# Optimization experiments

Hardware: AMD Instinct MI355X
Metric: run time of the kernel (lower is better)

Reference implementation:

```python
import jax, jax.numpy as jnp
import numpy as np

B, L, D = 2, 2048, 1024
H = 16          # num_heads == num_key_value_heads
FD = 16         # feature_dim (q/k head dim)
HD = D // H     # head_dim = 64 (v head dim)
EPS = 1e-5


def setup_inputs() -> dict:
    key = jax.random.key(0)
    k0, k1, k2, k3, k4 = jax.random.split(key, 5)
    scale = 0.02
    return {
        "hidden_states": jax.random.normal(k0, (B, L, D), jnp.float32),
        "Wq": jax.random.normal(k1, (D, H * FD), jnp.float32) * scale,
        "Wk": jax.random.normal(k2, (D, H * FD), jnp.float32) * scale,
        "Wv": jax.random.normal(k3, (D, H * HD), jnp.float32) * scale,
        "Wo": jax.random.normal(k4, (H * HD, D), jnp.float32) * scale,
    }


def reference(hidden_states, Wq, Wk, Wv, Wo):
    # projections (bias-free), split heads: b l (h d) -> b h l d
    q = (hidden_states @ Wq).reshape(B, L, H, FD).transpose(0, 2, 1, 3)
    k = (hidden_states @ Wk).reshape(B, L, H, FD).transpose(0, 2, 1, 3)
    v = (hidden_states @ Wv).reshape(B, L, H, HD).transpose(0, 2, 1, 3)

    # parallel_rebased: squared-dot-product kernel attention, causal,
    # row-normalized by the kernel sum (use_scale=True, use_normalize=True)
    qk_scale = FD ** -0.5
    s = jnp.einsum('bhqd,bhkd->bhqk', q * qk_scale, k)
    s = s * s  # quadratic feature map: (q.k)^2
    causal = jnp.tril(jnp.ones((L, L), dtype=bool))
    s = jnp.where(causal, s, 0.0)
    z = jnp.sum(s, axis=-1)  # [B,H,L]
    o = jnp.einsum('bhqk,bhkd->bhqd', s, v) / (z[..., None] + EPS)

    # merge heads: b h l d -> b l (h d), output projection
    o = o.transpose(0, 2, 1, 3).reshape(B, L, H * HD)
    return o @ Wo
```

## Files before the change

### kernel.cpp

```cpp
#include <hip/hip_runtime.h>
#include <hip/hip_bf16.h>

#define BB 2
#define LL 2048
#define DD 1024
#define HH 16
#define FD 16
#define HD 64
#define EPS 1e-5f
#define RQKV 1536
#define NFIX 4

typedef __attribute__((ext_vector_type(4))) float f32x4;
typedef __attribute__((ext_vector_type(8))) _Float16 f16x8;
typedef __attribute__((ext_vector_type(4))) _Float16 f16x4;
typedef __attribute__((ext_vector_type(4))) unsigned int u32x4;

__global__ __launch_bounds__(256) void prep(
    const float* __restrict__ Wq, const float* __restrict__ Wk,
    const float* __restrict__ Wv, const float* __restrict__ Wo,
    const float* __restrict__ hs, _Float16* __restrict__ WqkvT,
    _Float16* __restrict__ WoT, float* __restrict__ QKVe,
    _Float16* __restrict__ HS16) {
  __shared__ __attribute__((aligned(16))) char smem[40960];
  const int bx = blockIdx.x;
  const int tid = threadIdx.x;

  if (bx >= 2608) {
    int idx = ((bx - 2608) * 256 + tid) * 16;
#pragma unroll
    for (int half = 0; half < 2; half++) {
      float4 a = *(const float4*)(hs + idx + half * 8);
      float4 b = *(const float4*)(hs + idx + half * 8 + 4);
      f16x8 p = {(_Float16)a.x, (_Float16)a.y, (_Float16)a.z, (_Float16)a.w,
                 (_Float16)b.x, (_Float16)b.y, (_Float16)b.z, (_Float16)b.w};
      *(f16x8*)(HS16 + idx + half * 8) = p;
    }
    return;
  }

  if (bx < 2560) {
    _Float16(*s)[40] = (_Float16(*)[40])smem;
    const float* src;
    _Float16* dst;
    int n0, ncol, drow, k0;
    if (bx < 1536) {
      int ct = bx % 48, kt = bx / 48;
      if (ct < 8) { src = Wq; n0 = ct * 32; ncol = 256; drow = n0; }
      else if (ct < 16) { src = Wk; n0 = (ct - 8) * 32; ncol = 256; drow = 256 + n0; }
      else { src = Wv; n0 = (ct - 16) * 32; ncol = 1024; drow = 512 + n0; }
      k0 = kt * 32;
      dst = WqkvT;
    } else {
      int i2 = bx - 1536;
      n0 = (i2 & 31) * 32; k0 = (i2 >> 5) * 32;
      src = Wo; ncol = DD; drow = n0; dst = WoT;
    }
    {
      int r = tid >> 3, c = (tid & 7) * 4;
      float4 v = *(const float4*)(src + (size_t)(k0 + r) * ncol + n0 + c);
      f16x4 p = {(_Float16)v.x, (_Float16)v.y, (_Float16)v.z, (_Float16)v.w};
      *(f16x4*)&s[r][c] = p;
    }
    __syncthreads();
    {
      int n = tid >> 3, kk = (tid & 7) * 4;
      f16x4 o = {s[kk + 0][n], s[kk + 1][n], s[kk + 2][n], s[kk + 3][n]};
      *(f16x4*)(dst + (size_t)(drow + n) * DD + k0 + kk) = o;
    }
    return;
  }

  float(*sHS)[DD] = (float(*)[DD])smem;
  float(*part)[8][32] = (float(*)[8][32])(smem + 32768);
  const int kg = tid >> 5, c = tid & 31;
  const int c0 = (bx - 2560) * 32;

  for (int i = tid; i < 8 * (DD / 4); i += 256) {
    int e = i / (DD / 4), col4 = (i % (DD / 4)) * 4;
    int b = e >> 2, r = e & 3;
    *(float4*)&sHS[e][col4] =
        *(const float4*)(hs + (size_t)(b * LL + r) * DD + col4);
  }
  __syncthreads();

  const float* W;
  int col, ncol;
  if (c0 < 256) { W = Wq; col = c0 + c; ncol = 256; }
  else if (c0 < 512) { W = Wk; col = (c0 - 256) + c; ncol = 256; }
  else { W = Wv; col = (c0 - 512) + c; ncol = 1024; }

  float acc[8] = {};
  const int d0 = kg * 128;
#pragma unroll 4
  for (int d = d0; d < d0 + 128; d++) {
    float wv = W[(size_t)d * ncol + col];
#pragma unroll
    for (int e = 0; e < 8; e++) acc[e] += sHS[e][d] * wv;
  }
#pragma unroll
  for (int e = 0; e < 8; e++) part[kg][e][c] = acc[e];
  __syncthreads();

  {
    int e = tid >> 5;
    float t = 0.f;
#pragma unroll
    for (int g = 0; g < 8; g++) t += part[g][e][c];
    QKVe[(size_t)e * RQKV + c0 + c] = t;
  }
}

template <typename OutT>
__global__ __launch_bounds__(256) void gemm_f16(
    const _Float16* __restrict__ A, const _Float16* __restrict__ Bt,
    OutT* __restrict__ C, int M, int N, int K) {
  __shared__ __attribute__((aligned(16))) _Float16 sA[128 * 64];
  __shared__ __attribute__((aligned(16))) _Float16 sB[64 * 64];
  const int tid = threadIdx.x;
  const int m0 = blockIdx.y * 128, n0 = blockIdx.x * 64;
  const int w = tid >> 6, lane = tid & 63, quad = lane >> 4, l16 = lane & 15;
  const int wm = (w >> 1) * 64, wn = (w & 1) * 32;

  const int sr = tid >> 1, p = tid & 1;
  const int brow = (tid & 127) >> 1;
  const _Float16* Ag = A + (size_t)(m0 + sr) * K + p * 32;
  const _Float16* Bg = Bt + (size_t)(n0 + brow) * K + p * 32;
  _Float16* sAw = &sA[sr * 64];
  _Float16* sBw = &sB[brow * 64];
  const int aswz = sr & 7, bswz = brow & 7;

  f32x4 acc[4][2];
#pragma unroll
  for (int i = 0; i < 4; i++)
#pragma unroll
    for (int j = 0; j < 2; j++) acc[i][j] = (f32x4){0.f, 0.f, 0.f, 0.f};

  f16x8 ar[4], br[4];
  auto LOAD = [&](int k0) {
#pragma unroll
    for (int i = 0; i < 4; i++) ar[i] = *(const f16x8*)(Ag + k0 + i * 8);
    if (tid < 128) {
#pragma unroll
      for (int i = 0; i < 4; i++) br[i] = *(const f16x8*)(Bg + k0 + i * 8);
    }
  };
  LOAD(0);

  for (int k0 = 0; k0 < K; k0 += 64) {
    __syncthreads();
#pragma unroll
    for (int i = 0; i < 4; i++)
      *(f16x8*)(sAw + (((4 * p + i) ^ aswz) * 8)) = ar[i];
    if (tid < 128) {
#pragma unroll
      for (int i = 0; i < 4; i++)
        *(f16x8*)(sBw + (((4 * p + i) ^ bswz) * 8)) = br[i];
    }
    __syncthreads();
    if (k0 + 64 < K) LOAD(k0 + 64);

#pragma unroll
    for (int s = 0; s < 2; s++) {
      f16x8 af[4], bf[2];
#pragma unroll
      for (int i = 0; i < 4; i++) {
        int row = wm + i * 16 + l16;
        int col = ((s * 4 + quad) ^ (row & 7)) * 8;
        af[i] = *(const f16x8*)&sA[row * 64 + col];
      }
#pragma unroll
      for (int j = 0; j < 2; j++) {
        int row = wn + j * 16 + l16;
        int col = ((s * 4 + quad) ^ (row & 7)) * 8;
        bf[j] = *(const f16x8*)&sB[row * 64 + col];
      }
#pragma unroll
      for (int i = 0; i < 4; i++)
#pragma unroll
        for (int j = 0; j < 2; j++)
          acc[i][j] = __builtin_amdgcn_mfma_f32_16x16x32_f16(af[i], bf[j], acc[i][j], 0, 0, 0);
    }
  }

#pragma unroll
  for (int i = 0; i < 4; i++)
#pragma unroll
    for (int j = 0; j < 2; j++)
#pragma unroll
      for (int r = 0; r < 4; r++) {
        const int row = m0 + wm + i * 16 + quad * 4 + r;
        const int col = n0 + wn + j * 16 + l16;
        C[(size_t)row * N + col] = (OutT)acc[i][j][r];
      }
}

__device__ __forceinline__ unsigned pack_f16x2(float a, float b) {
  unsigned short ua = __builtin_bit_cast(unsigned short, (_Float16)a);
  unsigned short ub = __builtin_bit_cast(unsigned short, (_Float16)b);
  return (unsigned)ua | ((unsigned)ub << 16);
}

#define SK5 24
#define SV5 136

__global__ __launch_bounds__(256, 5) void attn_mfma7(
    const _Float16* __restrict__ QKV, _Float16* __restrict__ O) {
  __shared__ __attribute__((aligned(16))) _Float16 sK[128 * SK5];
  __shared__ __attribute__((aligned(16))) _Float16 sVt[80 * SV5];

  const int bh = blockIdx.x;
  const int b = bh >> 4, h = bh & 15;
  const int qt = 31 - blockIdx.y;
  const int tid = threadIdx.x;
  const int w = tid >> 6;
  const int lane = tid & 63;
  const int quad = lane >> 4;
  const int l16 = lane & 15;
  const int gq = qt * 64 + w * 16;

  const int pc = (lane & 32) | ((lane & 12) << 1) | ((lane & 16) >> 2) | (lane & 3);

  f16x8 qfrag = {};
  if (quad < 2) {
    qfrag = *(const f16x8*)(QKV +
        (size_t)(b * LL + gq + l16) * RQKV + h * FD + quad * 8);
    const _Float16 RT2 = (_Float16)1.41421356f;
#pragma unroll
    for (int i = 0; i < 8; i++) qfrag[i] = qfrag[i] * RT2;
  }

  for (int t = tid; t < 16 * SV5; t += 256) {
    int r = t / SV5, c = t % SV5;
    sVt[64 * SV5 + t] = (_Float16)((r == 0 && c < 128) ? 1.0f : 0.0f);
  }
  __syncthreads();
  const f16x8 zf0 = *(const f16x8*)&sVt[(64 + l16) * SV5 + quad * 8];
  const f16x8 zf1 = *(const f16x8*)&sVt[(64 + l16) * SV5 + 32 + quad * 8];

  f32x4 oacc[4];
  f32x4 zacc = (f32x4){0.f, 0.f, 0.f, 0.f};
#pragma unroll
  for (int nt = 0; nt < 4; nt++) oacc[nt] = (f32x4){0.f, 0.f, 0.f, 0.f};

  const int nst = qt + 1;
  const int nkt = (nst + 1) >> 1;

  const int krow = tid >> 1, kcol = (tid & 1) * 8;
  f16x8 kreg;
  f16x8 vreg0, vreg1, vreg2, vreg3;
  auto LOAD = [&](int kt) {
    kreg = *(const f16x8*)(QKV +
        (size_t)(b * LL + kt * 128 + krow) * RQKV + 256 + h * FD + kcol);
    const _Float16* vp = QKV +
        (size_t)(b * LL + kt * 128 + lane) * RQKV + 512 + h * HD + w * 16;
    vreg0 = *(const f16x8*)vp;
    vreg1 = *(const f16x8*)(vp + 8);
    vp += (size_t)64 * RQKV;
    vreg2 = *(const f16x8*)vp;
    vreg3 = *(const f16x8*)(vp + 8);
  };
  LOAD(0);

  for (int kt = 0; kt < nkt; kt++) {
    __syncthreads();
    *(f16x8*)&sK[krow * SK5 + kcol] = kreg;
#pragma unroll
    for (int t = 0; t < 8; t++) sVt[(w * 16 + t) * SV5 + pc] = vreg0[t];
#pragma unroll
    for (int t = 0; t < 8; t++) sVt[(w * 16 + 8 + t) * SV5 + pc] = vreg1[t];
#pragma unroll
    for (int t = 0; t < 8; t++) sVt[(w * 16 + t) * SV5 + 64 + pc] = vreg2[t];
#pragma unroll
    for (int t = 0; t < 8; t++) sVt[(w * 16 + 8 + t) * SV5 + 64 + pc] = vreg3[t];
    __syncthreads();
    if (kt + 1 < nkt) LOAD(kt + 1);

#pragma unroll
    for (int hf = 0; hf < 2; hf++) {
      const int st = 2 * kt + hf;
      if (st >= nst) break;
      const int k0 = st * 64;
      const bool mask = (st == qt);

      f16x8 kf[4];
#pragma unroll
      for (int nt = 0; nt < 4; nt++) {
        f16x8 f = {};
        if (quad < 2)
          f = *(const f16x8*)&sK[(hf * 64 + nt * 16 + l16) * SK5 + quad * 8];
        kf[nt] = f;
      }

      unsigned wp[4][2];
#pragma unroll
      for (int nt = 0; nt < 4; nt++) {
        f32x4 s = __builtin_amdgcn_mfma_f32_16x16x32_f16(
            kf[nt], qfrag, (f32x4){0.f, 0.f, 0.f, 0.f}, 0, 0, 0);
        float s0 = s[0] * s[0], s1 = s[1] * s[1];
        float s2 = s[2] * s[2], s3 = s[3] * s[3];
        if (mask) {
          const int gkb = k0 + nt * 16 + quad * 4;
          const int qg = gq + l16;
          if (gkb + 0 > qg) s0 = 0.f;
          if (gkb + 1 > qg) s1 = 0.f;
          if (gkb + 2 > qg) s2 = 0.f;
          if (gkb + 3 > qg) s3 = 0.f;
        }
        wp[nt][0] = pack_f16x2(s0, s1);
        wp[nt][1] = pack_f16x2(s2, s3);
      }

      u32x4 u0 = {wp[0][0], wp[0][1], wp[1][0], wp[1][1]};
      u32x4 u1 = {wp[2][0], wp[2][1], wp[3][0], wp[3][1]};
      f16x8 af0 = __builtin_bit_cast(f16x8, u0);
      f16x8 af1 = __builtin_bit_cast(f16x8, u1);

#pragma unroll
      for (int nt = 0; nt < 4; nt++) {
        f16x8 vf0 = *(const f16x8*)&sVt[(nt * 16 + l16) * SV5 + hf * 64 + quad * 8];
        f16x8 vf1 = *(const f16x8*)&sVt[(nt * 16 + l16) * SV5 + hf * 64 + 32 + quad * 8];
        oacc[nt] = __builtin_amdgcn_mfma_f32_16x16x32_f16(af0, vf0, oacc[nt], 0, 0, 0);
        oacc[nt] = __builtin_amdgcn_mfma_f32_16x16x32_f16(af1, vf1, oacc[nt], 0, 0, 0);
      }
      zacc = __builtin_amdgcn_mfma_f32_16x16x32_f16(af0, zf0, zacc, 0, 0, 0);
      zacc = __builtin_amdgcn_mfma_f32_16x16x32_f16(af1, zf1, zacc, 0, 0, 0);
    }
  }

  {
    float rz[4];
#pragma unroll
    for (int r = 0; r < 4; r++) {
      float zz = __shfl(zacc[r], lane & 48);
      rz[r] = 1.0f / (zz + 32.0f * EPS);
    }
#pragma unroll
    for (int nt = 0; nt < 4; nt++)
#pragma unroll
      for (int r = 0; r < 4; r++) {
        const int gqr = gq + quad * 4 + r;
        O[(size_t)(b * LL + gqr) * (HH * HD) + h * HD + nt * 16 + l16] =
            (_Float16)(oacc[nt][r] * rz[r]);
      }
  }
}

__global__ __launch_bounds__(256) void fix_final(
    const float* __restrict__ QKVe, _Float16* __restrict__ Oatt) {
  const int b = blockIdx.x >> 4, h = blockIdx.x & 15;
  const int tid = threadIdx.x;
  const int p = tid >> 6, d = tid & 63;

  float num = 0.f, z = 0.f;
  const float* qrow = QKVe + (size_t)(b * 4 + p) * RQKV + h * FD;
  for (int j = 0; j <= p; j++) {
    const float* krow = QKVe + (size_t)(b * 4 + j) * RQKV + 256 + h * FD;
    float s = 0.f;
#pragma unroll
    for (int f = 0; f < FD; f++) s += qrow[f] * krow[f];
    s *= 0.25f;
    s = s * s;
    z += s;
    num += s * QKVe[(size_t)(b * 4 + j) * RQKV + 512 + h * HD + d];
  }
  Oatt[(size_t)(b * LL + p) * (HH * HD) + h * HD + d] =
      (_Float16)(num / (z + EPS));
}

extern "C" void kernel_launch(void* const* d_in, const int* in_sizes, int n_in,
                              void* d_out, int out_size, void* d_ws, size_t ws_size,
                              hipStream_t stream) {
  const float* hs = (const float*)d_in[0];
  const float* Wq = (const float*)d_in[1];
  const float* Wk = (const float*)d_in[2];
  const float* Wv = (const float*)d_in[3];
  const float* Wo = (const float*)d_in[4];
  float* out = (float*)d_out;

  char* ws = (char*)d_ws;
  _Float16* WqkvT = (_Float16*)ws;
  _Float16* WoT   = (_Float16*)(ws + (3ull << 20));
  _Float16* HS16  = (_Float16*)(ws + (5ull << 20));
  _Float16* QKV   = (_Float16*)(ws + (13ull << 20));
  _Float16* Oatt  = (_Float16*)(ws + (25ull << 20));
  float*    QKVe  = (float*)(ws + (33ull << 20));

  const int M = BB * LL;

  prep<<<dim3(3632), 256, 0, stream>>>(Wq, Wk, Wv, Wo, hs, WqkvT, WoT, QKVe, HS16);

  gemm_f16<_Float16><<<dim3(RQKV / 64, M / 128), 256, 0, stream>>>(
      HS16, WqkvT, QKV, M, RQKV, DD);

  attn_mfma7<<<dim3(BB * HH, LL / 64), 256, 0, stream>>>(QKV, Oatt);

  fix_final<<<dim3(BB * HH), 256, 0, stream>>>(QKVe, Oatt);

  gemm_f16<float><<<dim3(DD / 64, M / 128), 256, 0, stream>>>(
      Oatt, WoT, out, M, DD, DD);
}
```

Baseline: 165.7 us.

## Pre-transpose V into a separate buffer so attention stores it to LDS with vector writes

Adds a `vtrans` kernel that transposes the V slice of the fused QKV buffer into a feature-major VT layout in workspace. The attention kernel then reads V rows that are already transposed and writes them to LDS with 8-byte stores through a permutation table. Previously each thread did 32 scalar 2-byte scattered LDS stores per tile. The aim is to cut LDS store instruction count and bank pressure in the attention main loop, at the cost of an extra kernel launch and an extra global read and write pass over V.

```diff
diff --git a/kernel.cpp b/kernel.cpp
--- a/kernel.cpp
+++ b/kernel.cpp
@@ -195,6 +195,34 @@
       }
 }
 
+__global__ __launch_bounds__(256) void vtrans(
+    const _Float16* __restrict__ QKV, _Float16* __restrict__ VT) {
+  __shared__ __attribute__((aligned(16))) _Float16 s[64][136];
+  const int h = blockIdx.x >> 5, tt = blockIdx.x & 31;
+  const int tid = threadIdx.x;
+
+  {
+    const int tok = tid >> 1, dh = (tid & 1) * 32;
+    const _Float16* src =
+        QKV + (size_t)(tt * 128 + tok) * RQKV + 512 + h * HD + dh;
+    f16x8 r[4];
+#pragma unroll
+    for (int i = 0; i < 4; i++) r[i] = *(const f16x8*)(src + i * 8);
+#pragma unroll
+    for (int i = 0; i < 4; i++)
+#pragma unroll
+      for (int e = 0; e < 8; e++) s[dh + i * 8 + e][tok] = r[i][e];
+  }
+  __syncthreads();
+  {
+    const int d = tid >> 2, ck = (tid & 3) * 32;
+    _Float16* dst = VT + (size_t)(h * HD + d) * (BB * LL) + tt * 128 + ck;
+#pragma unroll
+    for (int i = 0; i < 4; i++)
+      *(f16x8*)(dst + i * 8) = *(const f16x8*)&s[d][ck + i * 8];
+  }
+}
+
 __device__ __forceinline__ unsigned pack_f16x2(float a, float b) {
   unsigned short ua = __builtin_bit_cast(unsigned short, (_Float16)a);
   unsigned short ub = __builtin_bit_cast(unsigned short, (_Float16)b);
@@ -204,8 +232,9 @@
 #define SK5 24
 #define SV5 136
 
-__global__ __launch_bounds__(256, 5) void attn_mfma7(
-    const _Float16* __restrict__ QKV, _Float16* __restrict__ O) {
+__global__ __launch_bounds__(256, 5) void attn_mfma8(
+    const _Float16* __restrict__ QKV, const _Float16* __restrict__ VT,
+    _Float16* __restrict__ O) {
   __shared__ __attribute__((aligned(16))) _Float16 sK[128 * SK5];
   __shared__ __attribute__((aligned(16))) _Float16 sVt[80 * SV5];
 
@@ -219,8 +248,6 @@
   const int l16 = lane & 15;
   const int gq = qt * 64 + w * 16;
 
-  const int pc = (lane & 32) | ((lane & 12) << 1) | ((lane & 16) >> 2) | (lane & 3);
-
   f16x8 qfrag = {};
   if (quad < 2) {
     qfrag = *(const f16x8*)(QKV +
@@ -247,32 +274,36 @@
   const int nkt = (nst + 1) >> 1;
 
   const int krow = tid >> 1, kcol = (tid & 1) * 8;
+  const int vdrow = w * 16 + (lane >> 2);
+  const int vc0 = (lane & 3) * 32;
+  const _Float16* VTb =
+      VT + (size_t)(h * HD + vdrow) * (BB * LL) + b * LL + vc0;
   f16x8 kreg;
-  f16x8 vreg0, vreg1, vreg2, vreg3;
+  f16x8 vreg[4];
   auto LOAD = [&](int kt) {
     kreg = *(const f16x8*)(QKV +
         (size_t)(b * LL + kt * 128 + krow) * RQKV + 256 + h * FD + kcol);
-    const _Float16* vp = QKV +
-        (size_t)(b * LL + kt * 128 + lane) * RQKV + 512 + h * HD + w * 16;
-    vreg0 = *(const f16x8*)vp;
-    vreg1 = *(const f16x8*)(vp + 8);
-    vp += (size_t)64 * RQKV;
-    vreg2 = *(const f16x8*)vp;
-    vreg3 = *(const f16x8*)(vp + 8);
+    const _Float16* vp = VTb + kt * 128;
+#pragma unroll
+    for (int i = 0; i < 4; i++) vreg[i] = *(const f16x8*)(vp + i * 8);
   };
   LOAD(0);
 
   for (int kt = 0; kt < nkt; kt++) {
     __syncthreads();
     *(f16x8*)&sK[krow * SK5 + kcol] = kreg;
-#pragma unroll
-    for (int t = 0; t < 8; t++) sVt[(w * 16 + t) * SV5 + pc] = vreg0[t];
-#pragma unroll
-    for (int t = 0; t < 8; t++) sVt[(w * 16 + 8 + t) * SV5 + pc] = vreg1[t];
-#pragma unroll
-    for (int t = 0; t < 8; t++) sVt[(w * 16 + t) * SV5 + 64 + pc] = vreg2[t];
-#pragma unroll
-    for (int t = 0; t < 8; t++) sVt[(w * 16 + 8 + t) * SV5 + 64 + pc] = vreg3[t];
+    {
+      _Float16* sv = &sVt[vdrow * SV5 + vc0];
+#pragma unroll
+      for (int a = 0; a < 8; a++) {
+        constexpr int tab[8] = {0, 8, 16, 24, 4, 12, 20, 28};
+        u32x4 u = __builtin_bit_cast(u32x4, vreg[a >> 1]);
+        uint2 val;
+        val.x = u[2 * (a & 1)];
+        val.y = u[2 * (a & 1) + 1];
+        *(uint2*)(sv + tab[a]) = val;
+      }
+    }
     __syncthreads();
     if (kt + 1 < nkt) LOAD(kt + 1);
 
@@ -385,6 +416,7 @@
   _Float16* QKV   = (_Float16*)(ws + (13ull << 20));
   _Float16* Oatt  = (_Float16*)(ws + (25ull << 20));
   float*    QKVe  = (float*)(ws + (33ull << 20));
+  _Float16* VT    = (_Float16*)(ws + (34ull << 20));
 
   const int M = BB * LL;
 
@@ -393,7 +425,9 @@
   gemm_f16<_Float16><<<dim3(RQKV / 64, M / 128), 256, 0, stream>>>(
       HS16, WqkvT, QKV, M, RQKV, DD);
 
-  attn_mfma7<<<dim3(BB * HH, LL / 64), 256, 0, stream>>>(QKV, Oatt);
+  vtrans<<<dim3(512), 256, 0, stream>>>(QKV, VT);
+
+  attn_mfma8<<<dim3(BB * HH, LL / 64), 256, 0, stream>>>(QKV, VT, Oatt);
 
   fix_final<<<dim3(BB * HH), 256, 0, stream>>>(QKVe, Oatt);
 
```

Measured after the change: 167.2 us. No clear change (+0.9%).

## Fuse first-rows attention fixup into output GEMM and reorder attention tiles

Applied to the files above, without the earlier changes.

Removes the separate fix_final launch. The first four rows of each batch are now computed inside the output projection GEMM, which writes them directly into the shared-memory A tile per k-chunk, so the fixup no longer needs an extra kernel and a global round trip. It also changes the query-tile ordering in the attention kernel to interleave heavy and light causal tiles, aiming for better load balance. The cost is extra work and an extra sync in the two GEMM row-blocks that hold batch starts.

```diff
diff --git a/kernel.cpp b/kernel.cpp
--- a/kernel.cpp
+++ b/kernel.cpp
@@ -111,16 +111,48 @@
   }
 }
 
-template <typename OutT>
+template <typename OutT, bool FIXA>
 __global__ __launch_bounds__(256) void gemm_f16(
     const _Float16* __restrict__ A, const _Float16* __restrict__ Bt,
-    OutT* __restrict__ C, int M, int N, int K) {
+    OutT* __restrict__ C, int M, int N, int K,
+    const float* __restrict__ QKVe) {
   __shared__ __attribute__((aligned(16))) _Float16 sA[128 * 64];
   __shared__ __attribute__((aligned(16))) _Float16 sB[64 * 64];
+  __shared__ float sfx2[FIXA ? 16 * 4 * 4 : 1];
+  __shared__ float sfxz[FIXA ? 16 * 4 : 1];
   const int tid = threadIdx.x;
   const int m0 = blockIdx.y * 128, n0 = blockIdx.x * 64;
   const int w = tid >> 6, lane = tid & 63, quad = lane >> 4, l16 = lane & 15;
   const int wm = (w >> 1) * 64, wn = (w & 1) * 32;
+
+  int fixb = -1;
+  if constexpr (FIXA) {
+    if (m0 == 0) fixb = 0;
+    else if (m0 == LL) fixb = 1;
+    if (fixb >= 0) {
+      const int hh = tid >> 4, u = tid & 15;
+      if (u < 10) {
+        const int p = (u < 1) ? 0 : (u < 3) ? 1 : (u < 6) ? 2 : 3;
+        const int j = u - p * (p + 1) / 2;
+        const float* qrow = QKVe + (size_t)(fixb * 4 + p) * RQKV + hh * FD;
+        const float* krow = QKVe + (size_t)(fixb * 4 + j) * RQKV + 256 + hh * FD;
+        float s = 0.f;
+#pragma unroll
+        for (int f = 0; f < FD; f++) s += qrow[f] * krow[f];
+        s *= 0.25f;
+        sfx2[(hh * 4 + p) * 4 + j] = s * s;
+      }
+      __syncthreads();
+      if (tid < 64) {
+        const int hh2 = tid >> 2, p = tid & 3;
+        float z = 0.f;
+#pragma unroll
+        for (int j = 0; j < 4; j++)
+          if (j <= p) z += sfx2[(hh2 * 4 + p) * 4 + j];
+        sfxz[hh2 * 4 + p] = z;
+      }
+    }
+  }
 
   const int sr = tid >> 1, p = tid & 1;
   const int brow = (tid & 127) >> 1;
@@ -129,6 +161,7 @@
   _Float16* sAw = &sA[sr * 64];
   _Float16* sBw = &sB[brow * 64];
   const int aswz = sr & 7, bswz = brow & 7;
+  const bool skipA = FIXA && fixb >= 0 && sr < 4;
 
   f32x4 acc[4][2];
 #pragma unroll
@@ -149,13 +182,31 @@
 
   for (int k0 = 0; k0 < K; k0 += 64) {
     __syncthreads();
-#pragma unroll
-    for (int i = 0; i < 4; i++)
-      *(f16x8*)(sAw + (((4 * p + i) ^ aswz) * 8)) = ar[i];
+    if (!skipA) {
+#pragma unroll
+      for (int i = 0; i < 4; i++)
+        *(f16x8*)(sAw + (((4 * p + i) ^ aswz) * 8)) = ar[i];
+    }
     if (tid < 128) {
 #pragma unroll
       for (int i = 0; i < 4; i++)
         *(f16x8*)(sBw + (((4 * p + i) ^ bswz) * 8)) = br[i];
+    }
+    if constexpr (FIXA) {
+      if (fixb >= 0) {
+        const int pp = tid >> 6, cc = tid & 63;
+        const int hh = k0 >> 6;
+        float num = 0.f;
+#pragma unroll
+        for (int j = 0; j < 4; j++)
+          if (j <= pp)
+            num = fmaf(sfx2[(hh * 4 + pp) * 4 + j],
+                       QKVe[(size_t)(fixb * 4 + j) * RQKV + 512 + k0 + cc],
+                       num);
+        const float zz = sfxz[hh * 4 + pp];
+        sA[pp * 64 + (((cc >> 3) ^ pp) * 8) + (cc & 7)] =
+            (_Float16)(num / (zz + EPS));
+      }
     }
     __syncthreads();
     if (k0 + 64 < K) LOAD(k0 + 64);
@@ -204,14 +255,16 @@
 #define SK5 24
 #define SV5 136
 
-__global__ __launch_bounds__(256, 5) void attn_mfma7(
+__global__ __launch_bounds__(256, 5) void attn_mfma9(
     const _Float16* __restrict__ QKV, _Float16* __restrict__ O) {
   __shared__ __attribute__((aligned(16))) _Float16 sK[128 * SK5];
   __shared__ __attribute__((aligned(16))) _Float16 sVt[80 * SV5];
 
   const int bh = blockIdx.x;
   const int b = bh >> 4, h = bh & 15;
-  const int qt = 31 - blockIdx.y;
+  const int y = blockIdx.y;
+  const int qt = (y < 8) ? (31 - y) : (y < 16) ? (y + 8)
+               : (y < 24) ? (31 - y) : (y - 24);
   const int tid = threadIdx.x;
   const int w = tid >> 6;
   const int lane = tid & 63;
@@ -346,28 +399,6 @@
   }
 }
 
-__global__ __launch_bounds__(256) void fix_final(
-    const float* __restrict__ QKVe, _Float16* __restrict__ Oatt) {
-  const int b = blockIdx.x >> 4, h = blockIdx.x & 15;
-  const int tid = threadIdx.x;
-  const int p = tid >> 6, d = tid & 63;
-
-  float num = 0.f, z = 0.f;
-  const float* qrow = QKVe + (size_t)(b * 4 + p) * RQKV + h * FD;
-  for (int j = 0; j <= p; j++) {
-    const float* krow = QKVe + (size_t)(b * 4 + j) * RQKV + 256 + h * FD;
-    float s = 0.f;
-#pragma unroll
-    for (int f = 0; f < FD; f++) s += qrow[f] * krow[f];
-    s *= 0.25f;
-    s = s * s;
-    z += s;
-    num += s * QKVe[(size_t)(b * 4 + j) * RQKV + 512 + h * HD + d];
-  }
-  Oatt[(size_t)(b * LL + p) * (HH * HD) + h * HD + d] =
-      (_Float16)(num / (z + EPS));
-}
-
 extern "C" void kernel_launch(void* const* d_in, const int* in_sizes, int n_in,
                               void* d_out, int out_size, void* d_ws, size_t ws_size,
                               hipStream_t stream) {
@@ -390,13 +421,11 @@
 
   prep<<<dim3(3632), 256, 0, stream>>>(Wq, Wk, Wv, Wo, hs, WqkvT, WoT, QKVe, HS16);
 
-  gemm_f16<_Float16><<<dim3(RQKV / 64, M / 128), 256, 0, stream>>>(
-      HS16, WqkvT, QKV, M, RQKV, DD);
-
-  attn_mfma7<<<dim3(BB * HH, LL / 64), 256, 0, stream>>>(QKV, Oatt);
-
-  fix_final<<<dim3(BB * HH), 256, 0, stream>>>(QKVe, Oatt);
-
-  gemm_f16<float><<<dim3(DD / 64, M / 128), 256, 0, stream>>>(
-      Oatt, WoT, out, M, DD, DD);
+  gemm_f16<_Float16, false><<<dim3(RQKV / 64, M / 128), 256, 0, stream>>>(
+      HS16, WqkvT, QKV, M, RQKV, DD, nullptr);
+
+  attn_mfma9<<<dim3(BB * HH, LL / 64), 256, 0, stream>>>(QKV, Oatt);
+
+  gemm_f16<float, true><<<dim3(DD / 64, M / 128), 256, 0, stream>>>(
+      Oatt, WoT, out, M, DD, DD, QKVe);
 }
```

New measurement: 177.5 us. 1.07x slower.
